# Performance work log

Hardware: AMD Instinct MI355X
Metric: run time of the kernel (lower is better)

The kernel has to match this reference:

```python
import jax, jax.numpy as jnp
import numpy as np
from jax import lax

QMAX = 127.0  # symmetric int8 fake-quant levels
EPS = 1e-5    # batchnorm eps


def fq(x):
    """Per-tensor symmetric fake-quant with straight-through estimator.
    Simulates ChopSTE: round/clip to low precision in fwd, identity grad in bwd."""
    s = jnp.maximum(jnp.max(jnp.abs(x)) / QMAX, 1e-8)
    q = jnp.clip(jnp.round(x / s), -QMAX, QMAX) * s
    return x + lax.stop_gradient(q - x)


def conv2d(x, w, b):
    # NCHW input, OIHW kernel, padding=1 (SAME for 3x3)
    y = lax.conv_general_dilated(x, w, window_strides=(1, 1),
                                 padding=((1, 1), (1, 1)),
                                 dimension_numbers=('NCHW', 'OIHW', 'NCHW'))
    return y + b[None, :, None, None]


def maxpool2(x):
    return lax.reduce_window(x, -jnp.inf, lax.max, (1, 1, 2, 2), (1, 1, 2, 2), 'VALID')


def bn(x, g, be, m, v):
    inv = g / jnp.sqrt(v + EPS)  # [C]
    return x * inv[None, :, None, None] + (be - m * inv)[None, :, None, None]


def setup_inputs() -> dict:
    key = jax.random.key(0)
    ks = jax.random.split(key, 17)
    B = 8192
    d = {}
    d['x'] = jax.random.normal(ks[0], (B, 1, 28, 28), jnp.float32)
    d['w1'] = jax.random.normal(ks[1], (16, 1, 3, 3), jnp.float32) * 0.3
    d['b1'] = jax.random.normal(ks[2], (16,), jnp.float32) * 0.1
    d['g1'] = jax.random.uniform(ks[3], (16,), jnp.float32, 0.5, 1.5)
    d['be1'] = jax.random.normal(ks[4], (16,), jnp.float32) * 0.1
    d['m1'] = jax.random.normal(ks[5], (16,), jnp.float32) * 0.1
    d['v1'] = jax.random.uniform(ks[6], (16,), jnp.float32, 0.5, 1.5)
    d['w2'] = jax.random.normal(ks[7], (32, 16, 3, 3), jnp.float32) * 0.1
    d['b2'] = jax.random.normal(ks[8], (32,), jnp.float32) * 0.1
    d['g2'] = jax.random.uniform(ks[9], (32,), jnp.float32, 0.5, 1.5)
    d['be2'] = jax.random.normal(ks[10], (32,), jnp.float32) * 0.1
    d['m2'] = jax.random.normal(ks[11], (32,), jnp.float32) * 0.1
    d['v2'] = jax.random.uniform(ks[12], (32,), jnp.float32, 0.5, 1.5)
    d['fw1'] = jax.random.normal(ks[13], (128, 1568), jnp.float32) * 0.03
    d['fb1'] = jax.random.normal(ks[14], (128,), jnp.float32) * 0.1
    d['fw2'] = jax.random.normal(ks[15], (10, 128), jnp.float32) * 0.1
    d['fb2'] = jax.random.normal(ks[16], (10,), jnp.float32) * 0.1
    return d


def reference(x, w1, b1, g1, be1, m1, v1, w2, b2, g2, be2, m2, v2, fw1, fb1, fw2, fb2):
    # block 1: quantized conv -> quantized relu -> quantized bn -> maxpool
    h = fq(conv2d(x, fq(w1), b1))           # [B,16,28,28]
    h = fq(jax.nn.relu(h))
    h = fq(bn(h, g1, be1, m1, v1))
    h = maxpool2(h)                          # [B,16,14,14]
    # block 2
    h = fq(conv2d(h, fq(w2), b2))           # [B,32,14,14]
    h = fq(jax.nn.relu(h))
    h = fq(bn(h, g2, be2, m2, v2))
    h = maxpool2(h)                          # [B,32,7,7]
    # classifier (dropout is identity at inference)
    h = h.reshape(h.shape[0], -1)            # [B,1568]
    h = fq(h @ fq(fw1).T + fb1)              # [B,128]
    h = fq(jax.nn.relu(h))
    out = fq(h @ fq(fw2).T + fb2)            # [B,10]
    return out
```

## Files before the change

kernel.cpp:

```cpp
#include <hip/hip_runtime.h>
#include <math.h>
#include <limits.h>
#include <stdint.h>

#define QMAXF 127.0f
#define BN_EPS 1e-5f
#define NCOPIES 64

typedef int v4i __attribute__((ext_vector_type(4)));
typedef float f32x4 __attribute__((ext_vector_type(4)));
typedef _Float16 f16x8 __attribute__((ext_vector_type(8)));

__device__ __forceinline__ int f2ord(float f){
    int i = __float_as_int(f);
    return i ^ ((i >> 31) & 0x7fffffff);
}
__device__ __forceinline__ float ord2f(int i){
    return __int_as_float(i ^ ((i >> 31) & 0x7fffffff));
}
__device__ __forceinline__ float scale_of(float m){
    return fmaxf(m / QMAXF, 1e-8f);
}
__device__ __forceinline__ float fq_apply(float x, float s){
    float q = rintf(x / s);
    q = fminf(fmaxf(q, -QMAXF), QMAXF);
    return q * s;
}
__device__ __forceinline__ float quant_k(float x, float s){
    float q = rintf(x / s);
    return fminf(fmaxf(q, -QMAXF), QMAXF);
}
__device__ __forceinline__ _Float16 hpart(uint32_t w){
    return __builtin_bit_cast(_Float16, (unsigned short)(w >> 16));
}
__device__ __forceinline__ _Float16 lpart(uint32_t w){
    return __builtin_bit_cast(_Float16, (unsigned short)(w & 0xffffu));
}

__global__ __launch_bounds__(256) void k_init_ws(
    const float* __restrict__ w1, const float* __restrict__ w2,
    const float* __restrict__ fw1, const float* __restrict__ fw2,
    int* __restrict__ s1, int* __restrict__ s2, int* __restrict__ sf, int* __restrict__ so,
    float* __restrict__ wsbuf )
{
    int blk = blockIdx.x, t = threadIdx.x;
    if (blk < 26){
        int gt = blk*256 + t;
        if (gt < 2048){ int j = gt & 31; s1[gt] = (j < 16) ? INT_MAX : INT_MIN; }
        else if (gt < 6144){ int u = gt - 2048; int j = u & 63; s2[u] = (j < 32) ? INT_MAX : INT_MIN; }
        else if (gt < 6272){ int u = gt - 6144; sf[u] = ((u & 1) == 0) ? INT_MAX : INT_MIN; }
        else if (gt < 6400){ int u = gt - 6272; so[u] = ((u & 1) == 0) ? INT_MAX : INT_MIN; }
        return;
    }
    __shared__ float red[256];
    int b2 = blk - 26;
    const float* src; int n, base;
    if (b2 < 64){ src = fw1; base = b2*3136; n = 3136; }
    else if (b2 == 64){ src = w1;  base = 0; n = 144; }
    else if (b2 == 65){ src = w2;  base = 0; n = 4608; }
    else { src = fw2; base = 0; n = 1280; }
    float m = 0.f;
    for (int i = t; i < n; i += 256) m = fmaxf(m, fabsf(src[base + i]));
    red[t] = m; __syncthreads();
    for (int off = 128; off; off >>= 1){
        if (t < off) red[t] = fmaxf(red[t], red[t+off]);
        __syncthreads();
    }
    if (t == 0) wsbuf[b2] = red[0];
}

__global__ __launch_bounds__(256) void k_pack_prep(
    const float* __restrict__ x,
    const float* __restrict__ w1, const float* __restrict__ w2,
    const float* __restrict__ fw1, const float* __restrict__ fw2,
    const float* __restrict__ wsbuf,
    _Float16* __restrict__ wpk1h, int8_t* __restrict__ wpk2,
    int8_t* __restrict__ bpk1, float* __restrict__ qfw2,
    float* __restrict__ wscales, uint32_t* __restrict__ xp)
{
    int blk = blockIdx.x, t = threadIdx.x;
    if (blk >= 786){
        int i = (blk - 786)*256 + t;
        int b = i / 900, r = i - b*900;
        int yy = r / 30, xx = r - yy*30;
        float val = 0.f;
        if (yy >= 1 && yy <= 28 && xx >= 1 && xx <= 28)
            val = x[(size_t)b*784 + (yy-1)*28 + (xx-1)];
        _Float16 h  = (_Float16)val;
        _Float16 lo = (_Float16)(val - (float)h);
        xp[i] = ((uint32_t)__builtin_bit_cast(unsigned short, h) << 16)
              |  (uint32_t)__builtin_bit_cast(unsigned short, lo);
        return;
    }
    if (blk < 784){
        float m = 0.f;
        #pragma unroll
        for (int i = 0; i < 64; i++) m = fmaxf(m, wsbuf[i]);
        float s = scale_of(m);
        int i = blk*256 + t;
        int o = i / 1568, k = i - o*1568;
        int c = k / 49, r = k - c*49;
        int kp = r*32 + c;
        int kchunk = kp >> 6, rem = kp & 63, hi = rem >> 4, j = rem & 15;
        int code = (int)quant_k(fw1[i], s);
        bpk1[(o>>4)*25600 + (kchunk*4 + hi)*256 + (o&15)*16 + j] = (int8_t)code;
    } else if (blk == 784){
        float s0 = scale_of(wsbuf[64]), s3 = scale_of(wsbuf[66]);
        for (int i = t; i < 512; i += 256){
            int grp = i >> 3, j = i & 7;
            int hi = grp >> 4, col = grp & 15;
            _Float16 val = (_Float16)0.f;
            if (hi < 3){
                int jj = (j < 3) ? j : ((j < 6) ? (j - 3) : -1);
                if (jj >= 0) val = (_Float16)quant_k(w1[col*9 + hi*3 + jj], s0);
            }
            wpk1h[i] = val;
        }
        for (int i = t; i < 1280; i += 256) qfw2[i] = fq_apply(fw2[i], s3);
        for (int i = t; i < 4096; i += 256){
            int o = i >> 5, rem = (i & 31) + 32;
            int hi = rem >> 4, j = rem & 15;
            bpk1[(o>>4)*25600 + (24*4 + hi)*256 + (o&15)*16 + j] = 0;
        }
        if (t == 0){
            float m = 0.f;
            for (int i = 0; i < 64; i++) m = fmaxf(m, wsbuf[i]);
            wscales[0] = scale_of(wsbuf[64]);
            wscales[1] = scale_of(wsbuf[65]);
            wscales[2] = scale_of(m);
            wscales[3] = scale_of(wsbuf[66]);
        }
    } else {
        float s1 = scale_of(wsbuf[65]);
        for (int i = t; i < 6144; i += 256) wpk2[i] = 0;
        __syncthreads();
        for (int i = t; i < 4608; i += 256){
            int co = i / 144, rr = i - co*144, ci = rr / 9, pix = rr - ci*9;
            wpk2[(co >> 4)*3072 + pix*256 + (co & 15)*16 + ci] = (int8_t)(int)quant_k(w2[i], s1);
        }
    }
}

__device__ __forceinline__ f16x8 conv1_fragW(uint32_t w0, uint32_t w1, uint32_t w2)
{
    _Float16 z = (_Float16)0.f;
    return (f16x8){hpart(w0), hpart(w1), hpart(w2),
                   lpart(w0), lpart(w1), lpart(w2), z, z};
}

__global__ __launch_bounds__(256) void k_conv1s_mfma(
    const uint32_t* __restrict__ xp, const _Float16* __restrict__ wpk1h,
    const float* __restrict__ b1, const float* __restrict__ wscales,
    int* __restrict__ stats1)
{
    int t = threadIdx.x, l = t & 63, wid = t >> 6;
    int hi = l >> 4, col = l & 15;
    f16x8 bv = *(const f16x8*)(wpk1h + (hi*16 + col)*8);
    float sb = b1[col];
    float s0 = wscales[0];
    int tile0 = blockIdx.x*4 + wid;
    int p0 = tile0*16 + (l & 15);
    int b0 = p0 / 784, r = p0 - b0*784;
    int y = r / 28, xx = r - y*28;
    int rowo = (hi < 3) ? hi : 2;
    bool valid = hi < 3;
    const uint32_t* base = xp + (size_t)b0*900 + (y + rowo)*30 + xx;
    const size_t TS = (size_t)128*900;
    uint32_t n0[3], n1[3], n2[3], n3[3];
    if (valid){
        #pragma unroll
        for (int j = 0; j < 3; j++){
            n0[j] = base[j];           n1[j] = base[TS + j];
            n2[j] = base[2*TS + j];    n3[j] = base[3*TS + j];
        }
    } else {
        #pragma unroll
        for (int j = 0; j < 3; j++){ n0[j]=n1[j]=n2[j]=n3[j]=0u; }
    }
    float mn = INFINITY, mx = -INFINITY;
    #pragma unroll 1
    for (int it = 0; it < 16; it++){
        uint32_t w0[3], w1[3], w2[3], w3[3];
        #pragma unroll
        for (int j = 0; j < 3; j++){ w0[j]=n0[j]; w1[j]=n1[j]; w2[j]=n2[j]; w3[j]=n3[j]; }
        base += 4*TS;
        if (it < 15 && valid){
            #pragma unroll
            for (int j = 0; j < 3; j++){
                n0[j] = base[j];           n1[j] = base[TS + j];
                n2[j] = base[2*TS + j];    n3[j] = base[3*TS + j];
            }
        }
        f16x8 a0 = conv1_fragW(w0[0], w0[1], w0[2]);
        f16x8 a1 = conv1_fragW(w1[0], w1[1], w1[2]);
        f16x8 a2 = conv1_fragW(w2[0], w2[1], w2[2]);
        f16x8 a3 = conv1_fragW(w3[0], w3[1], w3[2]);
        f32x4 c0 = {0.f,0.f,0.f,0.f}, c1 = {0.f,0.f,0.f,0.f};
        f32x4 c2 = {0.f,0.f,0.f,0.f}, c3 = {0.f,0.f,0.f,0.f};
        c0 = __builtin_amdgcn_mfma_f32_16x16x32_f16(a0, bv, c0, 0, 0, 0);
        c1 = __builtin_amdgcn_mfma_f32_16x16x32_f16(a1, bv, c1, 0, 0, 0);
        c2 = __builtin_amdgcn_mfma_f32_16x16x32_f16(a2, bv, c2, 0, 0, 0);
        c3 = __builtin_amdgcn_mfma_f32_16x16x32_f16(a3, bv, c3, 0, 0, 0);
        #pragma unroll
        for (int rg = 0; rg < 4; rg++){
            mn = fminf(mn, fminf(fminf(c0[rg], c1[rg]), fminf(c2[rg], c3[rg])));
            mx = fmaxf(mx, fmaxf(fmaxf(c0[rg], c1[rg]), fmaxf(c2[rg], c3[rg])));
        }
    }
    mn = fmaf(s0, mn, sb);
    mx = fmaf(s0, mx, sb);
    mn = fminf(mn, __shfl_xor(mn, 16)); mn = fminf(mn, __shfl_xor(mn, 32));
    mx = fmaxf(mx, __shfl_xor(mx, 16)); mx = fmaxf(mx, __shfl_xor(mx, 32));
    if (l < 16){
        int* basep = stats1 + (blockIdx.x & (NCOPIES-1))*32;
        atomicMin(&basep[l],      f2ord(mn));
        atomicMax(&basep[16 + l], f2ord(mx));
    }
}

__global__ __launch_bounds__(256) void k_scales_block(
    const int* __restrict__ stats,
    const float* __restrict__ g, const float* __restrict__ be,
    const float* __restrict__ m, const float* __restrict__ v,
    float* __restrict__ s_out, int8_t* __restrict__ t1buf)
{
    __shared__ float cmn[16], cmx[16], invs[16], dds[16], sss[3];
    int t = threadIdx.x;
    if (t < 32){
        bool ismax = t >= 16; int c = t & 15;
        int acc = ismax ? INT_MIN : INT_MAX;
        for (int i = 0; i < NCOPIES; i++){
            int u = stats[i*32 + t];
            acc = ismax ? max(acc, u) : min(acc, u);
        }
        if (ismax) cmx[c] = ord2f(acc); else cmn[c] = ord2f(acc);
    }
    __syncthreads();
    if (t == 0){
        float am = 0.f;
        for (int c = 0; c < 16; c++) am = fmaxf(am, fmaxf(fabsf(cmn[c]), fabsf(cmx[c])));
        float sA_ = fmaxf(am / QMAXF, 1e-8f);
        float rmax = 0.f;
        float q1x[16], q1n[16];
        for (int c = 0; c < 16; c++){
            q1x[c] = fmaxf(fq_apply(cmx[c], sA_), 0.f);
            q1n[c] = fmaxf(fq_apply(cmn[c], sA_), 0.f);
            rmax = fmaxf(rmax, q1x[c]);
        }
        float sB_ = fmaxf(rmax / QMAXF, 1e-8f);
        float am3 = 0.f;
        for (int c = 0; c < 16; c++){
            float inv = g[c] / sqrtf(v[c] + BN_EPS);
            float dd  = be[c] - m[c]*inv;
            invs[c] = inv; dds[c] = dd;
            float ha = fmaf(fq_apply(q1x[c], sB_), inv, dd);
            float hb = fmaf(fq_apply(q1n[c], sB_), inv, dd);
            am3 = fmaxf(am3, fmaxf(fabsf(ha), fabsf(hb)));
        }
        float sC_ = fmaxf(am3 / QMAXF, 1e-8f);
        sss[0] = sA_; sss[1] = sB_; sss[2] = sC_;
        s_out[0] = sA_; s_out[1] = sB_; s_out[2] = sC_;
    }
    __syncthreads();
    float s1 = sss[0], s2 = sss[1], s3 = sss[2];
    for (int e = t; e < 2048; e += 256){
        int c = e >> 7, idx = e & 127;
        float hh = (float)idx * s1;
        float q2 = quant_k(hh, s2);
        float h2 = q2 * s2;
        float hb = fmaf(h2, invs[c], dds[c]);
        t1buf[e] = (int8_t)(int)quant_k(hb, s3);
    }
}

__global__ __launch_bounds__(256) void k_block1_mfma(
    const uint32_t* __restrict__ xp, const _Float16* __restrict__ wpk1h,
    const float* __restrict__ b1, const float* __restrict__ wscales,
    const float* __restrict__ scales, const int8_t* __restrict__ t1buf,
    int8_t* __restrict__ h1q)
{
    __shared__ int8_t T1l[16*132];
    int t = threadIdx.x, l = t & 63, wid = t >> 6;
    for (int e = t; e < 2048; e += 256)
        T1l[(e >> 7)*132 + (e & 127)] = t1buf[e];
    __syncthreads();
    int hi = l >> 4, col = l & 15;
    f16x8 bv = *(const f16x8*)(wpk1h + (hi*16 + col)*8);
    float sb = b1[col];
    float s0 = wscales[0], s1 = scales[0];
    int tile0 = blockIdx.x*4 + wid;
    int grow = tile0*16 + (l & 15);
    int cell = grow >> 2, sub = grow & 3;
    int b0 = cell / 196, rc = cell - b0*196;
    int py = rc / 14, px = rc - py*14;
    int y = 2*py + (sub >> 1), xx = 2*px + (sub & 1);
    int rowo = (hi < 3) ? hi : 2;
    bool valid = hi < 3;
    const uint32_t* base = xp + (size_t)b0*900 + (y + rowo)*30 + xx;
    const size_t TS = (size_t)512*900;
    const int8_t* T1c = T1l + col*132;
    int8_t* h1o = h1q + (size_t)tile0*64 + l;
    uint32_t n0[3], n1[3], n2[3], n3[3];
    if (valid){
        #pragma unroll
        for (int j = 0; j < 3; j++){
            n0[j] = base[j];           n1[j] = base[TS + j];
            n2[j] = base[2*TS + j];    n3[j] = base[3*TS + j];
        }
    } else {
        #pragma unroll
        for (int j = 0; j < 3; j++){ n0[j]=n1[j]=n2[j]=n3[j]=0u; }
    }
    #pragma unroll 1
    for (int it = 0; it < 4; it++){
        uint32_t w0[3], w1[3], w2[3], w3[3];
        #pragma unroll
        for (int j = 0; j < 3; j++){ w0[j]=n0[j]; w1[j]=n1[j]; w2[j]=n2[j]; w3[j]=n3[j]; }
        base += 4*TS;
        if (it < 3 && valid){
            #pragma unroll
            for (int j = 0; j < 3; j++){
                n0[j] = base[j];           n1[j] = base[TS + j];
                n2[j] = base[2*TS + j];    n3[j] = base[3*TS + j];
            }
        }
        f16x8 a0 = conv1_fragW(w0[0], w0[1], w0[2]);
        f16x8 a1 = conv1_fragW(w1[0], w1[1], w1[2]);
        f16x8 a2 = conv1_fragW(w2[0], w2[1], w2[2]);
        f16x8 a3 = conv1_fragW(w3[0], w3[1], w3[2]);
        f32x4 c0 = {0.f,0.f,0.f,0.f}, c1 = {0.f,0.f,0.f,0.f};
        f32x4 c2 = {0.f,0.f,0.f,0.f}, c3 = {0.f,0.f,0.f,0.f};
        c0 = __builtin_amdgcn_mfma_f32_16x16x32_f16(a0, bv, c0, 0, 0, 0);
        c1 = __builtin_amdgcn_mfma_f32_16x16x32_f16(a1, bv, c1, 0, 0, 0);
        c2 = __builtin_amdgcn_mfma_f32_16x16x32_f16(a2, bv, c2, 0, 0, 0);
        c3 = __builtin_amdgcn_mfma_f32_16x16x32_f16(a3, bv, c3, 0, 0, 0);
        float pool0 = fmaxf(fmaxf(c0[0], c0[1]), fmaxf(c0[2], c0[3]));
        float pool1 = fmaxf(fmaxf(c1[0], c1[1]), fmaxf(c1[2], c1[3]));
        float pool2 = fmaxf(fmaxf(c2[0], c2[1]), fmaxf(c2[2], c2[3]));
        float pool3 = fmaxf(fmaxf(c3[0], c3[1]), fmaxf(c3[2], c3[3]));
        float q0 = quant_k(fmaf(s0, pool0, sb), s1);
        float q1 = quant_k(fmaf(s0, pool1, sb), s1);
        float q2 = quant_k(fmaf(s0, pool2, sb), s1);
        float q3 = quant_k(fmaf(s0, pool3, sb), s1);
        h1o[0]                    = T1c[(int)fmaxf(q0, 0.f)];
        h1o[(size_t)100352*16]    = T1c[(int)fmaxf(q1, 0.f)];
        h1o[(size_t)2*100352*16]  = T1c[(int)fmaxf(q2, 0.f)];
        h1o[(size_t)3*100352*16]  = T1c[(int)fmaxf(q3, 0.f)];
        h1o += (size_t)4*100352*16;
    }
}

__global__ __launch_bounds__(256) void k_conv2s_mfma(
    const int8_t* __restrict__ h1q, const int8_t* __restrict__ wpk2,
    int* __restrict__ stats2)
{
    __shared__ int smn[32], smx[32];
    int t = threadIdx.x, l = t & 63, wid = t >> 6;
    if (t < 32){ smn[t] = INT_MAX; smx[t] = INT_MIN; }
    __syncthreads();
    int hi = l >> 4;
    v4i bv[6];
    #pragma unroll
    for (int nt = 0; nt < 2; nt++)
        #pragma unroll
        for (int s = 0; s < 3; s++)
            bv[nt*3+s] = *(const v4i*)(wpk2 + nt*3072 + (4*s + hi)*256 + (l&15)*16);
    int tile0 = blockIdx.x*4 + wid;
    int grow = tile0*16 + (l & 15);
    int cell_g = grow >> 2;
    int b0 = cell_g / 49, cell = cell_g - b0*49;
    int sub = grow & 3;
    int qy = cell / 7, qx = cell - qy*7;
    int y = 2*qy + (sub >> 1), x = 2*qx + (sub & 1);
    const int8_t* ip = h1q + (size_t)b0*196*16;
    int toff[3];
    #pragma unroll
    for (int s = 0; s < 3; s++){
        int tap = 4*s + hi;
        toff[s] = -1;
        if (tap < 9){
            int ky = tap / 3, kx = tap - ky*3;
            int yy = y + ky - 1, xc = x + kx - 1;
            if (yy >= 0 && yy < 14 && xc >= 0 && xc < 14)
                toff[s] = (yy*14 + xc)*16;
        }
    }
    v4i nav0 = (toff[0] >= 0) ? *(const v4i*)(ip + toff[0]) : (v4i){0,0,0,0};
    v4i nav1 = (toff[1] >= 0) ? *(const v4i*)(ip + toff[1]) : (v4i){0,0,0,0};
    v4i nav2 = (toff[2] >= 0) ? *(const v4i*)(ip + toff[2]) : (v4i){0,0,0,0};
    int mn0 = INT_MAX, mx0 = INT_MIN, mn1 = INT_MAX, mx1 = INT_MIN;
    #pragma unroll 1
    for (int it = 0; it < 16; it++){
        v4i av0 = nav0, av1 = nav1, av2 = nav2;
        ip += (size_t)512*196*16;
        if (it < 15){
            nav0 = (toff[0] >= 0) ? *(const v4i*)(ip + toff[0]) : (v4i){0,0,0,0};
            nav1 = (toff[1] >= 0) ? *(const v4i*)(ip + toff[1]) : (v4i){0,0,0,0};
            nav2 = (toff[2] >= 0) ? *(const v4i*)(ip + toff[2]) : (v4i){0,0,0,0};
        }
        v4i acc0 = (v4i){0,0,0,0}, acc1 = (v4i){0,0,0,0};
        acc0 = __builtin_amdgcn_mfma_i32_16x16x64_i8(av0, bv[0], acc0, 0, 0, 0);
        acc1 = __builtin_amdgcn_mfma_i32_16x16x64_i8(av0, bv[3], acc1, 0, 0, 0);
        acc0 = __builtin_amdgcn_mfma_i32_16x16x64_i8(av1, bv[1], acc0, 0, 0, 0);
        acc1 = __builtin_amdgcn_mfma_i32_16x16x64_i8(av1, bv[4], acc1, 0, 0, 0);
        acc0 = __builtin_amdgcn_mfma_i32_16x16x64_i8(av2, bv[2], acc0, 0, 0, 0);
        acc1 = __builtin_amdgcn_mfma_i32_16x16x64_i8(av2, bv[5], acc1, 0, 0, 0);
        #pragma unroll
        for (int r = 0; r < 4; r++){
            mn0 = min(mn0, acc0[r]); mx0 = max(mx0, acc0[r]);
            mn1 = min(mn1, acc1[r]); mx1 = max(mx1, acc1[r]);
        }
    }
    mn0 = min(mn0, __shfl_xor(mn0, 16)); mn0 = min(mn0, __shfl_xor(mn0, 32));
    mx0 = max(mx0, __shfl_xor(mx0, 16)); mx0 = max(mx0, __shfl_xor(mx0, 32));
    mn1 = min(mn1, __shfl_xor(mn1, 16)); mn1 = min(mn1, __shfl_xor(mn1, 32));
    mx1 = max(mx1, __shfl_xor(mx1, 16)); mx1 = max(mx1, __shfl_xor(mx1, 32));
    if (l < 16){
        atomicMin(&smn[l], mn0);      atomicMax(&smx[l], mx0);
        atomicMin(&smn[16 + l], mn1); atomicMax(&smx[16 + l], mx1);
    }
    __syncthreads();
    if (t < 32){
        int* basep = stats2 + (blockIdx.x & (NCOPIES-1))*64;
        atomicMin(&basep[t],      smn[t]);
        atomicMax(&basep[t + 32], smx[t]);
    }
}

__global__ __launch_bounds__(256) void k_scales2(
    const int* __restrict__ stats,
    const float* __restrict__ g, const float* __restrict__ be,
    const float* __restrict__ m, const float* __restrict__ v,
    const float* __restrict__ b2,
    const float* __restrict__ scales, const float* __restrict__ wscales,
    float* __restrict__ s_out, int8_t* __restrict__ t2buf)
{
    __shared__ float cmn[32], cmx[32], invs[32], dds[32], sss[3];
    int t = threadIdx.x;
    float S = scales[2] * wscales[1];
    if (t < 64){
        bool ismax = t >= 32; int c = t & 31;
        int acc = ismax ? INT_MIN : INT_MAX;
        for (int i = 0; i < NCOPIES; i++){
            int u = stats[i*64 + t];
            acc = ismax ? max(acc, u) : min(acc, u);
        }
        float val = fmaf(S, (float)acc, b2[c]);
        if (ismax) cmx[c] = val; else cmn[c] = val;
    }
    __syncthreads();
    if (t == 0){
        float am = 0.f;
        for (int c = 0; c < 32; c++) am = fmaxf(am, fmaxf(fabsf(cmn[c]), fabsf(cmx[c])));
        float sA_ = fmaxf(am / QMAXF, 1e-8f);
        float rmax = 0.f;
        float q1x[32], q1n[32];
        for (int c = 0; c < 32; c++){
            q1x[c] = fmaxf(fq_apply(cmx[c], sA_), 0.f);
            q1n[c] = fmaxf(fq_apply(cmn[c], sA_), 0.f);
            rmax = fmaxf(rmax, q1x[c]);
        }
        float sB_ = fmaxf(rmax / QMAXF, 1e-8f);
        float am3 = 0.f;
        for (int c = 0; c < 32; c++){
            float inv = g[c] / sqrtf(v[c] + BN_EPS);
            float dd  = be[c] - m[c]*inv;
            invs[c] = inv; dds[c] = dd;
            float ha = fmaf(fq_apply(q1x[c], sB_), inv, dd);
            float hb = fmaf(fq_apply(q1n[c], sB_), inv, dd);
            am3 = fmaxf(am3, fmaxf(fabsf(ha), fabsf(hb)));
        }
        float sC_ = fmaxf(am3 / QMAXF, 1e-8f);
        sss[0] = sA_; sss[1] = sB_; sss[2] = sC_;
        s_out[0] = sA_; s_out[1] = sB_; s_out[2] = sC_;
    }
    __syncthreads();
    float s4 = sss[0], s5 = sss[1], s6 = sss[2];
    for (int e = t; e < 4096; e += 256){
        int c = e >> 7, idx = e & 127;
        float hh = (float)idx * s4;
        float q5 = quant_k(hh, s5);
        float h2 = q5 * s5;
        float hb = fmaf(h2, invs[c], dds[c]);
        t2buf[e] = (int8_t)(int)quant_k(hb, s6);
    }
}

__global__ __launch_bounds__(256) void k_block2_mfma(
    const int8_t* __restrict__ h1q, const int8_t* __restrict__ wpk2,
    const float* __restrict__ b2, const float* __restrict__ scales,
    const float* __restrict__ wscales, const int8_t* __restrict__ t2buf,
    int8_t* __restrict__ h2q)
{
    __shared__ int8_t T2l[32*132];
    int t = threadIdx.x, l = t & 63, wid = t >> 6;
    for (int e = t; e < 4096; e += 256)
        T2l[(e >> 7)*132 + (e & 127)] = t2buf[e];
    __syncthreads();
    int hi = l >> 4, cl = l & 15;
    float S = scales[2] * wscales[1];
    float s4 = scales[3];
    float sb0 = b2[cl], sb1 = b2[16 + cl];
    const int8_t* T2a = T2l + cl*132;
    const int8_t* T2b = T2l + (16 + cl)*132;
    v4i bv[6];
    #pragma unroll
    for (int nt = 0; nt < 2; nt++)
        #pragma unroll
        for (int s = 0; s < 3; s++)
            bv[nt*3+s] = *(const v4i*)(wpk2 + nt*3072 + (4*s + hi)*256 + cl*16);
    int tile0 = blockIdx.x*4 + wid;
    int grow = tile0*16 + (l & 15);
    int cell_g = grow >> 2;
    int b0 = cell_g / 49, cell = cell_g - b0*49;
    int sub = grow & 3;
    int qy = cell / 7, qx = cell - qy*7;
    int y = 2*qy + (sub >> 1), x = 2*qx + (sub & 1);
    const int8_t* ip = h1q + (size_t)b0*196*16;
    int toff[3];
    #pragma unroll
    for (int s = 0; s < 3; s++){
        int tap = 4*s + hi;
        toff[s] = -1;
        if (tap < 9){
            int ky = tap / 3, kx = tap - ky*3;
            int yy = y + ky - 1, xc = x + kx - 1;
            if (yy >= 0 && yy < 14 && xc >= 0 && xc < 14)
                toff[s] = (yy*14 + xc)*16;
        }
    }
    v4i nav0 = (toff[0] >= 0) ? *(const v4i*)(ip + toff[0]) : (v4i){0,0,0,0};
    v4i nav1 = (toff[1] >= 0) ? *(const v4i*)(ip + toff[1]) : (v4i){0,0,0,0};
    v4i nav2 = (toff[2] >= 0) ? *(const v4i*)(ip + toff[2]) : (v4i){0,0,0,0};
    int8_t* h2o = h2q + (size_t)(tile0*4 + hi)*32 + cl;
    #pragma unroll 1
    for (int it = 0; it < 4; it++){
        v4i av0 = nav0, av1 = nav1, av2 = nav2;
        ip += (size_t)2048*196*16;
        if (it < 3){
            nav0 = (toff[0] >= 0) ? *(const v4i*)(ip + toff[0]) : (v4i){0,0,0,0};
            nav1 = (toff[1] >= 0) ? *(const v4i*)(ip + toff[1]) : (v4i){0,0,0,0};
            nav2 = (toff[2] >= 0) ? *(const v4i*)(ip + toff[2]) : (v4i){0,0,0,0};
        }
        v4i acc0 = (v4i){0,0,0,0}, acc1 = (v4i){0,0,0,0};
        acc0 = __builtin_amdgcn_mfma_i32_16x16x64_i8(av0, bv[0], acc0, 0, 0, 0);
        acc1 = __builtin_amdgcn_mfma_i32_16x16x64_i8(av0, bv[3], acc1, 0, 0, 0);
        acc0 = __builtin_amdgcn_mfma_i32_16x16x64_i8(av1, bv[1], acc0, 0, 0, 0);
        acc1 = __builtin_amdgcn_mfma_i32_16x16x64_i8(av1, bv[4], acc1, 0, 0, 0);
        acc0 = __builtin_amdgcn_mfma_i32_16x16x64_i8(av2, bv[2], acc0, 0, 0, 0);
        acc1 = __builtin_amdgcn_mfma_i32_16x16x64_i8(av2, bv[5], acc1, 0, 0, 0);
        int pool0 = max(max(acc0[0], acc0[1]), max(acc0[2], acc0[3]));
        int pool1 = max(max(acc1[0], acc1[1]), max(acc1[2], acc1[3]));
        float q0 = quant_k(fmaf(S, (float)pool0, sb0), s4);
        float q1 = quant_k(fmaf(S, (float)pool1, sb1), s4);
        h2o[0]  = T2a[(int)fmaxf(q0, 0.f)];
        h2o[16] = T2b[(int)fmaxf(q1, 0.f)];
        h2o += (size_t)100352*32;
    }
}

__global__ __launch_bounds__(256) void k_fc1(
    const int8_t* __restrict__ h2q, const int8_t* __restrict__ bpk1,
    const float* __restrict__ fb1, const float* __restrict__ scales,
    const float* __restrict__ wscales,
    float* __restrict__ fc1o, int* __restrict__ statsFc)
{
    __shared__ int smn, smx;
    int t = threadIdx.x, l = t & 63, wid = t >> 6;
    if (t == 0){ smn = INT_MAX; smx = INT_MIN; }
    __syncthreads();
    int wave_id = blockIdx.x*4 + wid;
    int mtile = wave_id >> 2;
    int quarter = wave_id & 3;
    int hi = l >> 4, lo = l & 15;
    const int8_t* arow = h2q + (size_t)(mtile*16 + lo)*1568;
    v4i acc[2];
    #pragma unroll
    for (int g = 0; g < 2; g++) acc[g] = (v4i){0,0,0,0};
    #pragma unroll 1
    for (int kc = 0; kc < 25; kc++){
        int koff = kc*64 + hi*16;
        v4i av = (v4i){0,0,0,0};
        if (koff < 1568) av = *(const v4i*)(arow + koff);
        #pragma unroll
        for (int g = 0; g < 2; g++){
            v4i bvv = *(const v4i*)(bpk1 + (quarter*2 + g)*25600 + (kc*4 + hi)*256 + lo*16);
            acc[g] = __builtin_amdgcn_mfma_i32_16x16x64_i8(av, bvv, acc[g], 0, 0, 0);
        }
    }
    float Sfc = scales[5] * wscales[2];
    float lmn = INFINITY, lmx = -INFINITY;
    #pragma unroll
    for (int g = 0; g < 2; g++){
        int o = (quarter*2 + g)*16 + lo;
        float bias = fb1[o];
        #pragma unroll
        for (int r = 0; r < 4; r++){
            int m = mtile*16 + hi*4 + r;
            float val = fmaf(Sfc, (float)acc[g][r], bias);
            fc1o[(size_t)m*128 + o] = val;
            lmn = fminf(lmn, val); lmx = fmaxf(lmx, val);
        }
    }
    #pragma unroll
    for (int d = 1; d < 64; d <<= 1){
        lmn = fminf(lmn, __shfl_xor(lmn, d));
        lmx = fmaxf(lmx, __shfl_xor(lmx, d));
    }
    if (l == 0){
        atomicMin(&smn, f2ord(lmn));
        atomicMax(&smx, f2ord(lmx));
    }
    __syncthreads();
    if (t == 0){
        int* basep = statsFc + (blockIdx.x & (NCOPIES-1))*2;
        atomicMin(&basep[0], smn); atomicMax(&basep[1], smx);
    }
}

__global__ __launch_bounds__(256) void k_fc2(
    const float* __restrict__ fc1o, const float* __restrict__ qfw2, const float* __restrict__ fb2,
    const int* __restrict__ statsFc, float* __restrict__ out, int* __restrict__ statsOut)
{
    __shared__ float sw[1280], sb2[10], Tf[128];
    __shared__ float s7sh, s8sh;
    __shared__ int smn, smx;
    int t = threadIdx.x;
    for (int i = t; i < 1280; i += 256) sw[i] = qfw2[i];
    if (t < 10) sb2[t] = fb2[t];
    if (t == 0){
        smn = INT_MAX; smx = INT_MIN;
        int mni = INT_MAX, mxi = INT_MIN;
        for (int i = 0; i < NCOPIES; i++){ mni = min(mni, statsFc[i*2]); mxi = max(mxi, statsFc[i*2+1]); }
        float mn = ord2f(mni), mx = ord2f(mxi);
        float am = fmaxf(fabsf(mn), fabsf(mx));
        float s7 = fmaxf(am / QMAXF, 1e-8f);
        float rmx = fmaxf(fq_apply(mx, s7), 0.f);
        s7sh = s7; s8sh = fmaxf(rmx / QMAXF, 1e-8f);
    }
    __syncthreads();
    float s7 = s7sh, s8 = s8sh;
    if (t < 128) Tf[t] = s8 * quant_k((float)t * s7, s8);
    __syncthreads();
    int b = blockIdx.x*256 + t;
    float acc[10];
    #pragma unroll
    for (int j = 0; j < 10; j++) acc[j] = sb2[j];
    const float* fp = fc1o + (size_t)b*128;
    for (int k = 0; k < 128; k += 4){
        float4 f = *(const float4*)(fp + k);
        float v0 = Tf[(int)fmaxf(quant_k(f.x, s7), 0.f)];
        float v1 = Tf[(int)fmaxf(quant_k(f.y, s7), 0.f)];
        float v2 = Tf[(int)fmaxf(quant_k(f.z, s7), 0.f)];
        float v3 = Tf[(int)fmaxf(quant_k(f.w, s7), 0.f)];
        #pragma unroll
        for (int j = 0; j < 10; j++){
            float a = acc[j];
            a = fmaf(v0, sw[j*128 + k],     a);
            a = fmaf(v1, sw[j*128 + k + 1], a);
            a = fmaf(v2, sw[j*128 + k + 2], a);
            a = fmaf(v3, sw[j*128 + k + 3], a);
            acc[j] = a;
        }
    }
    float lmn = INFINITY, lmx = -INFINITY;
    #pragma unroll
    for (int j = 0; j < 10; j++){
        out[(size_t)b*10 + j] = acc[j];
        lmn = fminf(lmn, acc[j]); lmx = fmaxf(lmx, acc[j]);
    }
    atomicMin(&smn, f2ord(lmn)); atomicMax(&smx, f2ord(lmx));
    __syncthreads();
    if (t == 0){
        int* basep = statsOut + (blockIdx.x & (NCOPIES-1))*2;
        atomicMin(&basep[0], smn); atomicMax(&basep[1], smx);
    }
}

__global__ void k_quant_out(float* __restrict__ out, const int* __restrict__ statsOut, int n){
    __shared__ float s9s;
    if (threadIdx.x == 0){
        int mni = INT_MAX, mxi = INT_MIN;
        for (int i = 0; i < NCOPIES; i++){ mni = min(mni, statsOut[i*2]); mxi = max(mxi, statsOut[i*2+1]); }
        float am = fmaxf(fabsf(ord2f(mni)), fabsf(ord2f(mxi)));
        s9s = fmaxf(am / QMAXF, 1e-8f);
    }
    __syncthreads();
    int i = blockIdx.x*256 + threadIdx.x;
    if (i < n) out[i] = fq_apply(out[i], s9s);
}

extern "C" void kernel_launch(void* const* d_in, const int* in_sizes, int n_in,
                              void* d_out, int out_size, void* d_ws, size_t ws_size,
                              hipStream_t stream)
{
    const float* x   = (const float*)d_in[0];
    const float* w1  = (const float*)d_in[1];
    const float* b1  = (const float*)d_in[2];
    const float* g1  = (const float*)d_in[3];
    const float* be1 = (const float*)d_in[4];
    const float* m1  = (const float*)d_in[5];
    const float* v1  = (const float*)d_in[6];
    const float* w2  = (const float*)d_in[7];
    const float* b2  = (const float*)d_in[8];
    const float* g2  = (const float*)d_in[9];
    const float* be2 = (const float*)d_in[10];
    const float* m2  = (const float*)d_in[11];
    const float* v2  = (const float*)d_in[12];
    const float* fw1 = (const float*)d_in[13];
    const float* fb1 = (const float*)d_in[14];
    const float* fw2 = (const float*)d_in[15];
    const float* fb2 = (const float*)d_in[16];
    float* out = (float*)d_out;

    char* ws = (char*)d_ws;
    size_t off = 0;
    auto alloc = [&](size_t bytes)->char*{
        char* p = ws + off;
        off = (off + bytes + 255) & ~(size_t)255;
        return p;
    };
    _Float16* wpk1h = (_Float16*)alloc(512*2);
    int8_t* wpk2  = (int8_t*)alloc(6144);
    int8_t* bpk1  = (int8_t*)alloc(204800);
    float* qfw2   = (float*)alloc(1280*4);
    float* scales = (float*)alloc(16*4);
    float* wscales= (float*)alloc(4*4);
    float* wsbuf  = (float*)alloc(67*4);
    int8_t* t1buf = (int8_t*)alloc(2048);
    int8_t* t2buf = (int8_t*)alloc(4096);
    int* stats1   = (int*)alloc(64*32*4);
    int* stats2   = (int*)alloc(64*64*4);
    int* statsFc  = (int*)alloc(64*2*4);
    int* statsOut = (int*)alloc(64*2*4);
    uint32_t* xp  = (uint32_t*)alloc((size_t)8192*900*4);
    int8_t* h1q   = (int8_t*)alloc((size_t)8192*196*16);
    int8_t* h2q   = (int8_t*)alloc((size_t)8192*49*32);
    float* fc1o   = (float*)alloc((size_t)8192*128*4);
    (void)ws_size;

    k_init_ws<<<93, 256, 0, stream>>>(w1, w2, fw1, fw2, stats1, stats2, statsFc, statsOut, wsbuf);
    k_pack_prep<<<29586, 256, 0, stream>>>(x, w1, w2, fw1, fw2, wsbuf, wpk1h, wpk2, bpk1, qfw2, wscales, xp);
    k_conv1s_mfma<<<1568, 256, 0, stream>>>(xp, wpk1h, b1, wscales, stats1);
    k_scales_block<<<1, 256, 0, stream>>>(stats1, g1, be1, m1, v1, scales + 0, t1buf);
    k_block1_mfma<<<6272, 256, 0, stream>>>(xp, wpk1h, b1, wscales, scales, t1buf, h1q);
    k_conv2s_mfma<<<1568, 256, 0, stream>>>(h1q, wpk2, stats2);
    k_scales2<<<1, 256, 0, stream>>>(stats2, g2, be2, m2, v2, b2, scales, wscales, scales + 3, t2buf);
    k_block2_mfma<<<6272, 256, 0, stream>>>(h1q, wpk2, b2, scales, wscales, t2buf, h2q);
    k_fc1<<<512, 256, 0, stream>>>(h2q, bpk1, fb1, scales, wscales, fc1o, statsFc);
    k_fc2<<<32, 256, 0, stream>>>(fc1o, qfw2, fb2, statsFc, out, statsOut);
    k_quant_out<<<320, 256, 0, stream>>>(out, statsOut, out_size);
}
```

Baseline: 181.9 us.

## Fuse conv2 stats/scales/block2 and FC tail into cooperative grid-synced kernels

Replaces the conv2 stats pass, the single-block scale kernel and the block2 recompute pass with one cooperative kernel. It keeps the pooled int32 conv results in registers and LDS across a grid sync, so h1q is read once instead of twice. It likewise fuses fc1, fc2 and the output quantization into one cooperative kernel with two grid syncs, removing the fc1o round-trip and several launches. In exchange it adds grid-wide sync cost, large per-thread register and LDS state, and lower occupancy. It also removes the software prefetch from the fallback conv2 kernels.

New measurement: 324.1 us. +78.2%, slower.

```diff
diff --git a/kernel.cpp b/kernel.cpp
--- a/kernel.cpp
+++ b/kernel.cpp
@@ -1,7 +1,10 @@
 #include <hip/hip_runtime.h>
+#include <hip/hip_cooperative_groups.h>
 #include <math.h>
 #include <limits.h>
 #include <stdint.h>
+
+namespace cg = cooperative_groups;
 
 #define QMAXF 127.0f
 #define BN_EPS 1e-5f
@@ -350,6 +353,275 @@
     }
 }
 
+__global__ __launch_bounds__(256, 4) void k_conv2_block2(
+    const int8_t* __restrict__ h1q, const int8_t* __restrict__ wpk2,
+    const float* __restrict__ b2,
+    float* __restrict__ scales, const float* __restrict__ wscales,
+    const float* __restrict__ g, const float* __restrict__ be,
+    const float* __restrict__ m, const float* __restrict__ v,
+    int* __restrict__ stats2, int8_t* __restrict__ h2q)
+{
+    __shared__ int plds[8192];
+    __shared__ int8_t T2l[32*132];
+    __shared__ int smn[32], smx[32];
+    __shared__ float cmn[32], cmx[32], invs[32], dds[32], sss[3];
+    int t = threadIdx.x, l = t & 63, wid = t >> 6;
+    if (t < 32){ smn[t] = INT_MAX; smx[t] = INT_MIN; }
+    __syncthreads();
+    int hi = l >> 4, cl = l & 15;
+    v4i bv[6];
+    #pragma unroll
+    for (int nt = 0; nt < 2; nt++)
+        #pragma unroll
+        for (int s = 0; s < 3; s++)
+            bv[nt*3+s] = *(const v4i*)(wpk2 + nt*3072 + (4*s + hi)*256 + cl*16);
+    int tile0 = blockIdx.x*4 + wid;
+    int grow = tile0*16 + (l & 15);
+    int cell_g = grow >> 2;
+    int b0 = cell_g / 49, cell = cell_g - b0*49;
+    int sub = grow & 3;
+    int qy = cell / 7, qx = cell - qy*7;
+    int y = 2*qy + (sub >> 1), x = 2*qx + (sub & 1);
+    const int8_t* ip = h1q + (size_t)b0*196*16;
+    int toff[3];
+    #pragma unroll
+    for (int s = 0; s < 3; s++){
+        int tap = 4*s + hi;
+        toff[s] = -1;
+        if (tap < 9){
+            int ky = tap / 3, kx = tap - ky*3;
+            int yy = y + ky - 1, xc = x + kx - 1;
+            if (yy >= 0 && yy < 14 && xc >= 0 && xc < 14)
+                toff[s] = (yy*14 + xc)*16;
+        }
+    }
+    int p0v[32];
+    int mn0 = INT_MAX, mx0 = INT_MIN, mn1 = INT_MAX, mx1 = INT_MIN;
+    #pragma unroll
+    for (int it = 0; it < 32; it++){
+        const int8_t* ipp = ip + (size_t)it*64*196*16;
+        v4i av0 = (toff[0] >= 0) ? *(const v4i*)(ipp + toff[0]) : (v4i){0,0,0,0};
+        v4i av1 = (toff[1] >= 0) ? *(const v4i*)(ipp + toff[1]) : (v4i){0,0,0,0};
+        v4i av2 = (toff[2] >= 0) ? *(const v4i*)(ipp + toff[2]) : (v4i){0,0,0,0};
+        v4i acc0 = (v4i){0,0,0,0}, acc1 = (v4i){0,0,0,0};
+        acc0 = __builtin_amdgcn_mfma_i32_16x16x64_i8(av0, bv[0], acc0, 0, 0, 0);
+        acc1 = __builtin_amdgcn_mfma_i32_16x16x64_i8(av0, bv[3], acc1, 0, 0, 0);
+        acc0 = __builtin_amdgcn_mfma_i32_16x16x64_i8(av1, bv[1], acc0, 0, 0, 0);
+        acc1 = __builtin_amdgcn_mfma_i32_16x16x64_i8(av1, bv[4], acc1, 0, 0, 0);
+        acc0 = __builtin_amdgcn_mfma_i32_16x16x64_i8(av2, bv[2], acc0, 0, 0, 0);
+        acc1 = __builtin_amdgcn_mfma_i32_16x16x64_i8(av2, bv[5], acc1, 0, 0, 0);
+        #pragma unroll
+        for (int r = 0; r < 4; r++){
+            mn0 = min(mn0, acc0[r]); mx0 = max(mx0, acc0[r]);
+            mn1 = min(mn1, acc1[r]); mx1 = max(mx1, acc1[r]);
+        }
+        p0v[it] = max(max(acc0[0], acc0[1]), max(acc0[2], acc0[3]));
+        plds[(wid*32 + it)*64 + l] = max(max(acc1[0], acc1[1]), max(acc1[2], acc1[3]));
+    }
+    mn0 = min(mn0, __shfl_xor(mn0, 16)); mn0 = min(mn0, __shfl_xor(mn0, 32));
+    mx0 = max(mx0, __shfl_xor(mx0, 16)); mx0 = max(mx0, __shfl_xor(mx0, 32));
+    mn1 = min(mn1, __shfl_xor(mn1, 16)); mn1 = min(mn1, __shfl_xor(mn1, 32));
+    mx1 = max(mx1, __shfl_xor(mx1, 16)); mx1 = max(mx1, __shfl_xor(mx1, 32));
+    if (l < 16){
+        atomicMin(&smn[l], mn0);      atomicMax(&smx[l], mx0);
+        atomicMin(&smn[16 + l], mn1); atomicMax(&smx[16 + l], mx1);
+    }
+    __syncthreads();
+    if (t < 32){
+        int* basep = stats2 + (blockIdx.x & (NCOPIES-1))*64;
+        atomicMin(&basep[t],      smn[t]);
+        atomicMax(&basep[t + 32], smx[t]);
+    }
+    __threadfence();
+    cg::this_grid().sync();
+    float S = scales[2] * wscales[1];
+    if (t < 64){
+        bool ismax = t >= 32; int c = t & 31;
+        int acc = ismax ? INT_MIN : INT_MAX;
+        for (int i = 0; i < NCOPIES; i++){
+            int u = stats2[i*64 + t];
+            acc = ismax ? max(acc, u) : min(acc, u);
+        }
+        float val = fmaf(S, (float)acc, b2[c]);
+        if (ismax) cmx[c] = val; else cmn[c] = val;
+    }
+    __syncthreads();
+    if (t == 0){
+        float am = 0.f;
+        for (int c = 0; c < 32; c++) am = fmaxf(am, fmaxf(fabsf(cmn[c]), fabsf(cmx[c])));
+        float sA_ = fmaxf(am / QMAXF, 1e-8f);
+        float rmax = 0.f;
+        float q1x[32], q1n[32];
+        for (int c = 0; c < 32; c++){
+            q1x[c] = fmaxf(fq_apply(cmx[c], sA_), 0.f);
+            q1n[c] = fmaxf(fq_apply(cmn[c], sA_), 0.f);
+            rmax = fmaxf(rmax, q1x[c]);
+        }
+        float sB_ = fmaxf(rmax / QMAXF, 1e-8f);
+        float am3 = 0.f;
+        for (int c = 0; c < 32; c++){
+            float inv = g[c] / sqrtf(v[c] + BN_EPS);
+            float dd  = be[c] - m[c]*inv;
+            invs[c] = inv; dds[c] = dd;
+            float ha = fmaf(fq_apply(q1x[c], sB_), inv, dd);
+            float hb = fmaf(fq_apply(q1n[c], sB_), inv, dd);
+            am3 = fmaxf(am3, fmaxf(fabsf(ha), fabsf(hb)));
+        }
+        float sC_ = fmaxf(am3 / QMAXF, 1e-8f);
+        sss[0] = sA_; sss[1] = sB_; sss[2] = sC_;
+        if (blockIdx.x == 0){ scales[3] = sA_; scales[4] = sB_; scales[5] = sC_; }
+    }
+    __syncthreads();
+    float s4 = sss[0], s5 = sss[1], s6 = sss[2];
+    for (int e = t; e < 4096; e += 256){
+        int c = e >> 7, idx = e & 127;
+        float hh = (float)idx * s4;
+        float q5 = quant_k(hh, s5);
+        float h2 = q5 * s5;
+        float hb = fmaf(h2, invs[c], dds[c]);
+        T2l[c*132 + idx] = (int8_t)(int)quant_k(hb, s6);
+    }
+    __syncthreads();
+    float sb0 = b2[cl], sb1 = b2[16 + cl];
+    const int8_t* T2a = T2l + cl*132;
+    const int8_t* T2b = T2l + (16 + cl)*132;
+    int8_t* h2o = h2q + (size_t)(tile0*4 + hi)*32 + cl;
+    #pragma unroll
+    for (int it = 0; it < 32; it++){
+        float q0 = quant_k(fmaf(S, (float)p0v[it], sb0), s4);
+        int pv1 = plds[(wid*32 + it)*64 + l];
+        float q1 = quant_k(fmaf(S, (float)pv1, sb1), s4);
+        h2o[0]  = T2a[(int)fmaxf(q0, 0.f)];
+        h2o[16] = T2b[(int)fmaxf(q1, 0.f)];
+        h2o += (size_t)12544*32;
+    }
+}
+
+__global__ __launch_bounds__(256, 2) void k_fc_tail(
+    const int8_t* __restrict__ h2q, const int8_t* __restrict__ bpk1,
+    const float* __restrict__ fb1, const float* __restrict__ scales,
+    const float* __restrict__ wscales,
+    const float* __restrict__ qfw2, const float* __restrict__ fb2,
+    float* __restrict__ out, int* __restrict__ statsFc, int* __restrict__ statsOut)
+{
+    __shared__ float fcl[16*132];
+    __shared__ float sw[1280], Tf[128];
+    __shared__ float s7sh, s8sh, s9sh;
+    __shared__ int smn, smx;
+    int t = threadIdx.x, l = t & 63, wid = t >> 6;
+    if (t == 0){ smn = INT_MAX; smx = INT_MIN; }
+    __syncthreads();
+    int hi = l >> 4, lo = l & 15;
+    const int8_t* arow = h2q + (size_t)(blockIdx.x*16 + lo)*1568;
+    v4i acc[2];
+    #pragma unroll
+    for (int gq = 0; gq < 2; gq++) acc[gq] = (v4i){0,0,0,0};
+    #pragma unroll 1
+    for (int kc = 0; kc < 25; kc++){
+        int koff = kc*64 + hi*16;
+        v4i av = (v4i){0,0,0,0};
+        if (koff < 1568) av = *(const v4i*)(arow + koff);
+        #pragma unroll
+        for (int gq = 0; gq < 2; gq++){
+            v4i bvv = *(const v4i*)(bpk1 + (wid*2 + gq)*25600 + (kc*4 + hi)*256 + lo*16);
+            acc[gq] = __builtin_amdgcn_mfma_i32_16x16x64_i8(av, bvv, acc[gq], 0, 0, 0);
+        }
+    }
+    float Sfc = scales[5] * wscales[2];
+    float lmn = INFINITY, lmx = -INFINITY;
+    #pragma unroll
+    for (int gq = 0; gq < 2; gq++){
+        int o = (wid*2 + gq)*16 + lo;
+        float bias = fb1[o];
+        #pragma unroll
+        for (int r = 0; r < 4; r++){
+            int lr = hi*4 + r;
+            float val = fmaf(Sfc, (float)acc[gq][r], bias);
+            fcl[lr*132 + o] = val;
+            lmn = fminf(lmn, val); lmx = fmaxf(lmx, val);
+        }
+    }
+    #pragma unroll
+    for (int d = 1; d < 64; d <<= 1){
+        lmn = fminf(lmn, __shfl_xor(lmn, d));
+        lmx = fmaxf(lmx, __shfl_xor(lmx, d));
+    }
+    if (l == 0){
+        atomicMin(&smn, f2ord(lmn));
+        atomicMax(&smx, f2ord(lmx));
+    }
+    __syncthreads();
+    if (t == 0){
+        int* basep = statsFc + (blockIdx.x & (NCOPIES-1))*2;
+        atomicMin(&basep[0], smn); atomicMax(&basep[1], smx);
+    }
+    __threadfence();
+    cg::this_grid().sync();
+    for (int i = t; i < 1280; i += 256) sw[i] = qfw2[i];
+    if (t == 0){
+        int mni = INT_MAX, mxi = INT_MIN;
+        for (int i = 0; i < NCOPIES; i++){ mni = min(mni, statsFc[i*2]); mxi = max(mxi, statsFc[i*2+1]); }
+        float mn = ord2f(mni), mx = ord2f(mxi);
+        float am = fmaxf(fabsf(mn), fabsf(mx));
+        float s7 = fmaxf(am / QMAXF, 1e-8f);
+        float rmx = fmaxf(fq_apply(mx, s7), 0.f);
+        s7sh = s7; s8sh = fmaxf(rmx / QMAXF, 1e-8f);
+        smn = INT_MAX; smx = INT_MIN;
+    }
+    __syncthreads();
+    float s7 = s7sh, s8 = s8sh;
+    if (t < 128) Tf[t] = s8 * quant_k((float)t * s7, s8);
+    __syncthreads();
+    if (t < 16){
+        float acc2[10];
+        #pragma unroll
+        for (int j = 0; j < 10; j++) acc2[j] = fb2[j];
+        const float* fp = fcl + t*132;
+        for (int k = 0; k < 128; k += 4){
+            float4 f = *(const float4*)(fp + k);
+            float v0 = Tf[(int)fmaxf(quant_k(f.x, s7), 0.f)];
+            float v1 = Tf[(int)fmaxf(quant_k(f.y, s7), 0.f)];
+            float v2 = Tf[(int)fmaxf(quant_k(f.z, s7), 0.f)];
+            float v3 = Tf[(int)fmaxf(quant_k(f.w, s7), 0.f)];
+            #pragma unroll
+            for (int j = 0; j < 10; j++){
+                float a = acc2[j];
+                a = fmaf(v0, sw[j*128 + k],     a);
+                a = fmaf(v1, sw[j*128 + k + 1], a);
+                a = fmaf(v2, sw[j*128 + k + 2], a);
+                a = fmaf(v3, sw[j*128 + k + 3], a);
+                acc2[j] = a;
+            }
+        }
+        int b = blockIdx.x*16 + t;
+        float pmn = INFINITY, pmx = -INFINITY;
+        #pragma unroll
+        for (int j = 0; j < 10; j++){
+            out[(size_t)b*10 + j] = acc2[j];
+            pmn = fminf(pmn, acc2[j]); pmx = fmaxf(pmx, acc2[j]);
+        }
+        atomicMin(&smn, f2ord(pmn)); atomicMax(&smx, f2ord(pmx));
+    }
+    __syncthreads();
+    if (t == 0){
+        int* basep = statsOut + (blockIdx.x & (NCOPIES-1))*2;
+        atomicMin(&basep[0], smn); atomicMax(&basep[1], smx);
+    }
+    __threadfence();
+    cg::this_grid().sync();
+    if (t == 0){
+        int mni = INT_MAX, mxi = INT_MIN;
+        for (int i = 0; i < NCOPIES; i++){ mni = min(mni, statsOut[i*2]); mxi = max(mxi, statsOut[i*2+1]); }
+        float am = fmaxf(fabsf(ord2f(mni)), fabsf(ord2f(mxi)));
+        s9sh = fmaxf(am / QMAXF, 1e-8f);
+    }
+    __syncthreads();
+    if (t < 160){
+        int i = blockIdx.x*160 + t;
+        out[i] = fq_apply(out[i], s9sh);
+    }
+}
+
 __global__ __launch_bounds__(256) void k_conv2s_mfma(
     const int8_t* __restrict__ h1q, const int8_t* __restrict__ wpk2,
     int* __restrict__ stats2)
@@ -385,19 +657,13 @@
                 toff[s] = (yy*14 + xc)*16;
         }
     }
-    v4i nav0 = (toff[0] >= 0) ? *(const v4i*)(ip + toff[0]) : (v4i){0,0,0,0};
-    v4i nav1 = (toff[1] >= 0) ? *(const v4i*)(ip + toff[1]) : (v4i){0,0,0,0};
-    v4i nav2 = (toff[2] >= 0) ? *(const v4i*)(ip + toff[2]) : (v4i){0,0,0,0};
     int mn0 = INT_MAX, mx0 = INT_MIN, mn1 = INT_MAX, mx1 = INT_MIN;
     #pragma unroll 1
     for (int it = 0; it < 16; it++){
-        v4i av0 = nav0, av1 = nav1, av2 = nav2;
+        v4i av0 = (toff[0] >= 0) ? *(const v4i*)(ip + toff[0]) : (v4i){0,0,0,0};
+        v4i av1 = (toff[1] >= 0) ? *(const v4i*)(ip + toff[1]) : (v4i){0,0,0,0};
+        v4i av2 = (toff[2] >= 0) ? *(const v4i*)(ip + toff[2]) : (v4i){0,0,0,0};
         ip += (size_t)512*196*16;
-        if (it < 15){
-            nav0 = (toff[0] >= 0) ? *(const v4i*)(ip + toff[0]) : (v4i){0,0,0,0};
-            nav1 = (toff[1] >= 0) ? *(const v4i*)(ip + toff[1]) : (v4i){0,0,0,0};
-            nav2 = (toff[2] >= 0) ? *(const v4i*)(ip + toff[2]) : (v4i){0,0,0,0};
-        }
         v4i acc0 = (v4i){0,0,0,0}, acc1 = (v4i){0,0,0,0};
         acc0 = __builtin_amdgcn_mfma_i32_16x16x64_i8(av0, bv[0], acc0, 0, 0, 0);
         acc1 = __builtin_amdgcn_mfma_i32_16x16x64_i8(av0, bv[3], acc1, 0, 0, 0);
@@ -529,19 +795,13 @@
                 toff[s] = (yy*14 + xc)*16;
         }
     }
-    v4i nav0 = (toff[0] >= 0) ? *(const v4i*)(ip + toff[0]) : (v4i){0,0,0,0};
-    v4i nav1 = (toff[1] >= 0) ? *(const v4i*)(ip + toff[1]) : (v4i){0,0,0,0};
-    v4i nav2 = (toff[2] >= 0) ? *(const v4i*)(ip + toff[2]) : (v4i){0,0,0,0};
     int8_t* h2o = h2q + (size_t)(tile0*4 + hi)*32 + cl;
     #pragma unroll 1
     for (int it = 0; it < 4; it++){
-        v4i av0 = nav0, av1 = nav1, av2 = nav2;
+        v4i av0 = (toff[0] >= 0) ? *(const v4i*)(ip + toff[0]) : (v4i){0,0,0,0};
+        v4i av1 = (toff[1] >= 0) ? *(const v4i*)(ip + toff[1]) : (v4i){0,0,0,0};
+        v4i av2 = (toff[2] >= 0) ? *(const v4i*)(ip + toff[2]) : (v4i){0,0,0,0};
         ip += (size_t)2048*196*16;
-        if (it < 3){
-            nav0 = (toff[0] >= 0) ? *(const v4i*)(ip + toff[0]) : (v4i){0,0,0,0};
-            nav1 = (toff[1] >= 0) ? *(const v4i*)(ip + toff[1]) : (v4i){0,0,0,0};
-            nav2 = (toff[2] >= 0) ? *(const v4i*)(ip + toff[2]) : (v4i){0,0,0,0};
-        }
         v4i acc0 = (v4i){0,0,0,0}, acc1 = (v4i){0,0,0,0};
         acc0 = __builtin_amdgcn_mfma_i32_16x16x64_i8(av0, bv[0], acc0, 0, 0, 0);
         acc1 = __builtin_amdgcn_mfma_i32_16x16x64_i8(av0, bv[3], acc1, 0, 0, 0);
@@ -739,15 +999,34 @@
     float* fc1o   = (float*)alloc((size_t)8192*128*4);
     (void)ws_size;
 
+    int mb1 = 0, mb2 = 0;
+    hipOccupancyMaxActiveBlocksPerMultiprocessor(&mb1, k_conv2_block2, 256, 0);
+    hipOccupancyMaxActiveBlocksPerMultiprocessor(&mb2, k_fc_tail, 256, 0);
+    bool coop1 = (mb1 * 256 >= 784);
+    bool coop2 = (mb2 * 256 >= 512);
+
     k_init_ws<<<93, 256, 0, stream>>>(w1, w2, fw1, fw2, stats1, stats2, statsFc, statsOut, wsbuf);
     k_pack_prep<<<29586, 256, 0, stream>>>(x, w1, w2, fw1, fw2, wsbuf, wpk1h, wpk2, bpk1, qfw2, wscales, xp);
     k_conv1s_mfma<<<1568, 256, 0, stream>>>(xp, wpk1h, b1, wscales, stats1);
     k_scales_block<<<1, 256, 0, stream>>>(stats1, g1, be1, m1, v1, scales + 0, t1buf);
     k_block1_mfma<<<6272, 256, 0, stream>>>(xp, wpk1h, b1, wscales, scales, t1buf, h1q);
-    k_conv2s_mfma<<<1568, 256, 0, stream>>>(h1q, wpk2, stats2);
-    k_scales2<<<1, 256, 0, stream>>>(stats2, g2, be2, m2, v2, b2, scales, wscales, scales + 3, t2buf);
-    k_block2_mfma<<<6272, 256, 0, stream>>>(h1q, wpk2, b2, scales, wscales, t2buf, h2q);
-    k_fc1<<<512, 256, 0, stream>>>(h2q, bpk1, fb1, scales, wscales, fc1o, statsFc);
-    k_fc2<<<32, 256, 0, stream>>>(fc1o, qfw2, fb2, statsFc, out, statsOut);
-    k_quant_out<<<320, 256, 0, stream>>>(out, statsOut, out_size);
-}
+    if (coop1){
+        void* args[] = {(void*)&h1q, (void*)&wpk2, (void*)&b2, (void*)&scales, (void*)&wscales,
+                        (void*)&g2, (void*)&be2, (void*)&m2, (void*)&v2,
+                        (void*)&stats2, (void*)&h2q};
+        hipLaunchCooperativeKernel((void*)k_conv2_block2, dim3(784), dim3(256), args, 0, stream);
+    } else {
+        k_conv2s_mfma<<<1568, 256, 0, stream>>>(h1q, wpk2, stats2);
+        k_scales2<<<1, 256, 0, stream>>>(stats2, g2, be2, m2, v2, b2, scales, wscales, scales + 3, t2buf);
+        k_block2_mfma<<<6272, 256, 0, stream>>>(h1q, wpk2, b2, scales, wscales, t2buf, h2q);
+    }
+    if (coop2){
+        void* args[] = {(void*)&h2q, (void*)&bpk1, (void*)&fb1, (void*)&scales, (void*)&wscales,
+                        (void*)&qfw2, (void*)&fb2, (void*)&out, (void*)&statsFc, (void*)&statsOut};
+        hipLaunchCooperativeKernel((void*)k_fc_tail, dim3(512), dim3(256), args, 0, stream);
+    } else {
+        k_fc1<<<512, 256, 0, stream>>>(h2q, bpk1, fb1, scales, wscales, fc1o, statsFc);
+        k_fc2<<<32, 256, 0, stream>>>(fc1o, qfw2, fb2, statsFc, out, statsOut);
+        k_quant_out<<<320, 256, 0, stream>>>(out, statsOut, out_size);
+    }
+}
```
